# Optimization experiments

Measured on AMD Instinct MI355X. Metric: run time of the kernel, lower is better.

Reference implementation:

```python
import jax, jax.numpy as jnp
import numpy as np

B, F, D, V = 8192, 26, 32, 100000
H1, H2 = 128, 128  # cin_size
U1, U2 = 400, 400  # dnn hidden units


def setup_inputs() -> dict:
    key = jax.random.key(0)
    ks = jax.random.split(key, 12)
    s = 0.05  # keep activations/sigmoid in a sane range
    return {
        "dense_inputs": jax.random.normal(ks[0], (B, 13), jnp.float32),
        "sparse_inputs": jax.random.randint(ks[1], (B, F), 0, V, jnp.int32),
        "E": jax.random.normal(ks[2], (F, V, D), jnp.float32) * s,
        "W_cin0": jax.random.normal(ks[3], (F, F, H1), jnp.float32) * s,
        "W_cin1": jax.random.normal(ks[4], (F, H1, H2), jnp.float32) * s,
        "W1": jax.random.normal(ks[5], (F * D, U1), jnp.float32) * s,
        "b1": jnp.zeros((U1,), jnp.float32),
        "W2": jax.random.normal(ks[6], (U1, U2), jnp.float32) * s,
        "b2": jnp.zeros((U2,), jnp.float32),
        "w_lin": jax.random.normal(ks[7], (F, 1), jnp.float32) * s,
        "b_lin": jnp.zeros((1,), jnp.float32),
        "w_out": jax.random.normal(ks[8], (1 + H1 + H2 + U2 + 13, 1), jnp.float32) * s,
        "b_out": jnp.zeros((1,), jnp.float32),
    }


def reference(dense_inputs, sparse_inputs, E, W_cin0, W_cin1, W1, b1, W2, b2,
              w_lin, b_lin, w_out, b_out):
    # Linear part: Dense(1) applied to raw (cast) sparse ids, as in the TF code.
    linear_out = sparse_inputs.astype(jnp.float32) @ w_lin + b_lin  # [B,1]

    # Embedding lookup: per-field tables. embed[b,f,:] = E[f, sparse[b,f], :]
    embed = E[jnp.arange(F)[None, :], sparse_inputs]  # [B,F,D]

    # CIN. The split->matmul->reshape->conv1d chain is exactly:
    #   x_{k+1}[b,h,d] = sum_{i,j} W_k[i,j,h] * X0[b,i,d] * x_k[b,j,d]
    X0 = embed
    x1 = jnp.einsum('bid,bjd,ijh->bhd', X0, X0, W_cin0)   # [B,H1,D]
    x2 = jnp.einsum('bid,bjd,ijh->bhd', X0, x1, W_cin1)   # [B,H2,D]
    cin_out = jnp.concatenate([x1, x2], axis=1).sum(axis=-1)  # [B,H1+H2]

    # DNN on flattened embeddings (dropout rate 0 -> identity at inference).
    v = embed.reshape(B, F * D)
    h = jax.nn.relu(v @ W1 + b1)
    h = jax.nn.relu(h @ W2 + b2)  # [B,U2]

    total = jnp.concatenate([linear_out, cin_out, h, dense_inputs], axis=-1)
    return jax.nn.sigmoid(total @ w_out + b_out)  # [B,1]
```

## Files before the change

kernel.cpp:

```cpp
#include <hip/hip_runtime.h>
#include <hip/hip_bf16.h>
#include <math.h>

typedef __attribute__((ext_vector_type(8))) short bf16x8;
typedef __attribute__((ext_vector_type(4))) float f32x4;

#define B_ 8192
#define F_ 26
#define D_ 32
#define V_ 100000

static const size_t OFF_VB   = 0;
static const size_t OFF_FD0  = 13631488;
static const size_t OFF_PDH2 = 13664256;
static const size_t OFF_H1B  = 13795328;
static const size_t OFF_W1T  = 20348928;
static const size_t OFF_W2T  = 21014528;
static const size_t OFF_MTF  = 21334528;
static const size_t OFF_K2T  = 21350912;

static __device__ __forceinline__ unsigned short f2b(float f) {
    unsigned int u = __float_as_uint(f);
    return (unsigned short)((u + 0x7FFF + ((u >> 16) & 1)) >> 16);
}
static __device__ __forceinline__ unsigned short f2bt(float f) {
    return (unsigned short)(__float_as_uint(f) >> 16);
}
static __device__ __forceinline__ unsigned int pk2t(float a, float b) {
    return __builtin_amdgcn_perm(__float_as_uint(b), __float_as_uint(a), 0x07060302u);
}
static __device__ __forceinline__ float bf2f(unsigned short u) {
    return __uint_as_float(((unsigned int)u) << 16);
}

static __device__ __forceinline__ void transpose_body(
    const float* __restrict__ src, unsigned short* __restrict__ dst,
    int K, int N, int bx, int by)
{
    __shared__ float tl[32][33];
    const int lx = threadIdx.x & 31, ly = threadIdx.x >> 5;
    const int n0 = bx * 32, k0 = by * 32;
#pragma unroll
    for (int i = 0; i < 4; ++i) {
        int k = k0 + ly + i * 8, n = n0 + lx;
        if (k < K && n < N) tl[ly + i * 8][lx] = src[(size_t)k * N + n];
    }
    __syncthreads();
#pragma unroll
    for (int i = 0; i < 4; ++i) {
        int n = n0 + ly + i * 8, k = k0 + lx;
        if (k < K && n < N) dst[(size_t)n * K + k] = f2b(tl[lx][ly + i * 8]);
    }
}

__global__ __launch_bounds__(256) void k0a(
    const float* __restrict__ W1, const float* __restrict__ W2,
    const float* __restrict__ Wc1, const float* __restrict__ wout,
    unsigned short* __restrict__ W1t, unsigned short* __restrict__ W2t,
    float* __restrict__ MtF)
{
    __shared__ float w2s[128];
    int bid = blockIdx.x;
    if (bid < 338) { transpose_body(W1, W1t, 832, 400, bid % 13, bid / 13); return; }
    bid -= 338;
    if (bid < 169) { transpose_body(W2, W2t, 400, 400, bid % 13, bid / 13); return; }
    bid -= 169;
    if (threadIdx.x < 128) w2s[threadIdx.x] = wout[129 + threadIdx.x];
    __syncthreads();
    int g = bid * 256 + threadIdx.x;
    int i = g >> 7, j = g & 127;
    float s = 0.f;
    if (i < F_) {
        const float* row = Wc1 + ((size_t)i * 128 + j) * 128;
        for (int h = 0; h < 128; h += 4) {
            float4 a = *(const float4*)(row + h);
            s = fmaf(a.x, w2s[h], s);
            s = fmaf(a.y, w2s[h + 1], s);
            s = fmaf(a.z, w2s[h + 2], s);
            s = fmaf(a.w, w2s[h + 3], s);
        }
    } else if (i == F_) {
        s = wout[1 + j];
    }
    MtF[g] = s;
}

__global__ __launch_bounds__(256) void k0b(
    const float* __restrict__ W0, const float* __restrict__ MtF,
    unsigned short* __restrict__ K2T)
{
    int g = blockIdx.x * 256 + threadIdx.x;
    int q = g >> 5, i = g & 31;
    float s = 0.f;
    if (q < 351) {
        int a = 0, base = 0;
        while (base + (F_ - a) <= q) { base += F_ - a; ++a; }
        int b = a + (q - base);
        const float* r0 = W0 + ((size_t)a * F_ + b) * 128;
        const float* r1 = W0 + ((size_t)b * F_ + a) * 128;
        const float* m  = MtF + (size_t)i * 128;
        if (a == b) {
            for (int j = 0; j < 128; j += 4) {
                float4 w = *(const float4*)(r0 + j);
                float4 mm = *(const float4*)(m + j);
                s += w.x * mm.x + w.y * mm.y + w.z * mm.z + w.w * mm.w;
            }
        } else {
            for (int j = 0; j < 128; j += 4) {
                float4 w = *(const float4*)(r0 + j);
                float4 w1 = *(const float4*)(r1 + j);
                float4 mm = *(const float4*)(m + j);
                s += (w.x + w1.x) * mm.x + (w.y + w1.y) * mm.y
                   + (w.z + w1.z) * mm.z + (w.w + w1.w) * mm.w;
            }
        }
    }
    unsigned short hi = f2b(s);
    float lo = s - bf2f(hi);
    K2T[g] = hi;
    K2T[11264 + g] = f2b(lo);
}

__global__ __launch_bounds__(256) void k1_embed_cin(
    const int*   __restrict__ sparse,
    const float* __restrict__ E,
    const unsigned short* __restrict__ K2T,
    const float* __restrict__ wlin,
    const float* __restrict__ blin,
    const float* __restrict__ wout,
    unsigned short* __restrict__ vb,
    float* __restrict__ fdot0)
{
    __shared__ __align__(16) unsigned short embT[32][40];
    __shared__ unsigned int PQ[352];
    __shared__ int idxs[F_];
    __shared__ float red[4];

    const int b = blockIdx.x, t = threadIdx.x;
    float cind = 0.f;

    if (t < F_) {
        int id = sparse[b * F_ + t];
        idxs[t] = id;
        cind = (float)id * wlin[t] * wout[0];
        int base = F_ * t - (t * (t - 1)) / 2;
        for (int j = t; j < F_; ++j)
            PQ[base + j - t] = (unsigned)t | ((unsigned)j << 16);
    }
    if (t == F_) PQ[351] = 0u;
    if (t >= 32 && t < 64) {
        int d = t - 32;
        embT[d][26] = 0x3F80;
        embT[d][27] = 0; embT[d][28] = 0; embT[d][29] = 0;
        embT[d][30] = 0; embT[d][31] = 0;
    }
    __syncthreads();

    if (t < 208) {
        int f = t >> 3, q = t & 7;
        float4 v4 = *(const float4*)(E + ((size_t)f * V_ + idxs[f]) * D_ + q * 4);
        uint2 uu; uu.x = pk2t(v4.x, v4.y); uu.y = pk2t(v4.z, v4.w);
        *(uint2*)(vb + (size_t)b * 832 + f * 32 + q * 4) = uu;
        embT[q * 4 + 0][f] = f2bt(v4.x);
        embT[q * 4 + 1][f] = f2bt(v4.y);
        embT[q * 4 + 2][f] = f2bt(v4.z);
        embT[q * 4 + 3][f] = f2bt(v4.w);
    }
    __syncthreads();

    const int wave = t >> 6, lane = t & 63;
    const int lr = lane & 15, lg = lane >> 4;
    const int mt = wave & 1;
    const int nb = wave >> 1;
    bf16x8 af = *(const bf16x8*)&embT[mt * 16 + lr][lg * 8];
    const unsigned short* ebase = &embT[mt * 16 + lg * 4][0];
    const unsigned short* Kb = K2T + (size_t)lr * 32 + lg * 8;

#pragma unroll
    for (int s = 0; s < 11; ++s) {
        const int nt = 2 * s + nb;
        bf16x8 bh = *(const bf16x8*)(Kb + (size_t)nt * 512);
        bf16x8 bl = *(const bf16x8*)(Kb + 11264 + (size_t)nt * 512);
        f32x4 h = {};
        h = __builtin_amdgcn_mfma_f32_16x16x32_bf16(af, bl, h, 0, 0, 0);
        h = __builtin_amdgcn_mfma_f32_16x16x32_bf16(af, bh, h, 0, 0, 0);
        unsigned pq = PQ[nt * 16 + lr];
        int oi = (int)(pq & 0xFFFFu), oj = (int)(pq >> 16);
#pragma unroll
        for (int r = 0; r < 4; ++r) {
            float ei = bf2f(ebase[r * 40 + oi]);
            float ej = bf2f(ebase[r * 40 + oj]);
            cind = fmaf(ei * ej, h[r], cind);
        }
    }

#pragma unroll
    for (int off = 1; off <= 32; off <<= 1) cind += __shfl_xor(cind, off, 64);
    if (lane == 0) red[wave] = cind;
    __syncthreads();
    if (t == 0) fdot0[b] = red[0] + red[1] + red[2] + red[3] + blin[0] * wout[0];
}

static __device__ __forceinline__ void gemm_core(
    const unsigned short* __restrict__ A, int lda,
    const unsigned short* __restrict__ Bt, int ldb, int N,
    int m0, int n0, int kbase, int kend,
    unsigned short (*As)[40], unsigned short (*Bs)[40],
    f32x4 (*acc)[2])
{
    const int t = threadIdx.x;
    const int wave = t >> 6, lane = t & 63;
    const int lr = lane & 15, lg = lane >> 4;
    const int wn = wave * 32;
    const int ar = t >> 2, kg = (t & 3) * 8;

    const unsigned short* aptr = A  + (size_t)(m0 + ar) * lda + kbase + kg;
    const unsigned short* bp0  = Bt + (size_t)(n0 + ar) * ldb + kbase + kg;
    const unsigned short* bp1  = Bt + (size_t)(n0 + 64 + ar) * ldb + kbase + kg;
    const bool bn0 = (n0 + ar) < N, bn1 = (n0 + 64 + ar) < N;
    const uint4 z4 = make_uint4(0u, 0u, 0u, 0u);
    const int nkt = (kend - kbase + 31) >> 5;
    uint4 av, bv0, bv1;
    {
        int k = kbase + kg;
        av  = (k < kend)        ? *(const uint4*)aptr : z4;
        bv0 = (bn0 && k < kend) ? *(const uint4*)bp0  : z4;
        bv1 = (bn1 && k < kend) ? *(const uint4*)bp1  : z4;
    }
    for (int kt = 0; kt < nkt; ++kt) {
        *(uint4*)&As[ar][kg]      = av;
        *(uint4*)&Bs[ar][kg]      = bv0;
        *(uint4*)&Bs[64 + ar][kg] = bv1;
        __syncthreads();
        if (kt + 1 < nkt) {
            int kn = kbase + (kt + 1) * 32 + kg;
            av  = (kn < kend)        ? *(const uint4*)(aptr + (kt + 1) * 32) : z4;
            bv0 = (bn0 && kn < kend) ? *(const uint4*)(bp0  + (kt + 1) * 32) : z4;
            bv1 = (bn1 && kn < kend) ? *(const uint4*)(bp1  + (kt + 1) * 32) : z4;
        }
        bf16x8 af[4], bfr[2];
#pragma unroll
        for (int i = 0; i < 4; ++i) af[i]  = *(const bf16x8*)&As[i * 16 + lr][lg * 8];
#pragma unroll
        for (int j = 0; j < 2; ++j) bfr[j] = *(const bf16x8*)&Bs[wn + j * 16 + lr][lg * 8];
#pragma unroll
        for (int i = 0; i < 4; ++i)
#pragma unroll
            for (int j = 0; j < 2; ++j)
                acc[i][j] = __builtin_amdgcn_mfma_f32_16x16x32_bf16(af[i], bfr[j], acc[i][j], 0, 0, 0);
        __syncthreads();
    }
}

__global__ __launch_bounds__(256) void k2_h1(
    const unsigned short* __restrict__ vb, const unsigned short* __restrict__ W1t,
    const float* __restrict__ b1, unsigned short* __restrict__ h1b)
{
    __shared__ __align__(16) unsigned short As[64][40];
    __shared__ __align__(16) unsigned short Bs[128][40];
    const int t = threadIdx.x;
    const int wave = t >> 6, lane = t & 63;
    const int lr = lane & 15, lg = lane >> 4;
    const int m0 = blockIdx.y * 64, n0 = blockIdx.x * 128;
    f32x4 acc[4][2] = {};
    gemm_core(vb, 832, W1t, 832, 400, m0, n0, 0, 832, As, Bs, acc);
#pragma unroll
    for (int i = 0; i < 4; ++i) {
        int mrow = m0 + i * 16 + lg * 4;
#pragma unroll
        for (int j = 0; j < 2; ++j) {
            int col = n0 + wave * 32 + j * 16 + lr;
            if (col >= 400) continue;
            float bb = b1[col];
#pragma unroll
            for (int r = 0; r < 4; ++r)
                h1b[(size_t)(mrow + r) * 400 + col] = f2bt(fmaxf(acc[i][j][r] + bb, 0.f));
        }
    }
}

__global__ __launch_bounds__(256) void k2_h2(
    const unsigned short* __restrict__ h1b, const unsigned short* __restrict__ W2t,
    const float* __restrict__ b2, const float* __restrict__ wout,
    float* __restrict__ pdh2)
{
    __shared__ __align__(16) unsigned short As[64][40];
    __shared__ __align__(16) unsigned short Bs[128][40];
    __shared__ float red[4][64];
    const int t = threadIdx.x;
    const int wave = t >> 6, lane = t & 63;
    const int lr = lane & 15, lg = lane >> 4;
    const int m0 = blockIdx.y * 64, n0 = blockIdx.x * 128;
    f32x4 acc[4][2] = {};
    gemm_core(h1b, 400, W2t, 400, 400, m0, n0, 0, 400, As, Bs, acc);
    float v[4][4];
#pragma unroll
    for (int i = 0; i < 4; ++i)
#pragma unroll
        for (int r = 0; r < 4; ++r) {
            float s = 0.f;
#pragma unroll
            for (int j = 0; j < 2; ++j) {
                int col = n0 + wave * 32 + j * 16 + lr;
                if (col < 400)
                    s = fmaf(fmaxf(acc[i][j][r] + b2[col], 0.f), wout[257 + col], s);
            }
#pragma unroll
            for (int off = 1; off <= 8; off <<= 1) s += __shfl_xor(s, off, 64);
            v[i][r] = s;
        }
    if (lr == 0) {
#pragma unroll
        for (int i = 0; i < 4; ++i)
#pragma unroll
            for (int r = 0; r < 4; ++r) red[wave][i * 16 + lg * 4 + r] = v[i][r];
    }
    __syncthreads();
    if (t < 64) pdh2[(size_t)blockIdx.x * B_ + m0 + t] = red[0][t] + red[1][t] + red[2][t] + red[3][t];
}

__global__ __launch_bounds__(256) void k3_final(
    const float* __restrict__ fdot0,
    const float* __restrict__ pdh2,
    const float* __restrict__ dense,
    const float* __restrict__ wout,
    const float* __restrict__ bout,
    float* __restrict__ out)
{
    const int b = blockIdx.x * 256 + threadIdx.x;
    float s = fdot0[b];
#pragma unroll
    for (int z = 0; z < 4; ++z) s += pdh2[(size_t)z * B_ + b];
#pragma unroll
    for (int q = 0; q < 13; ++q) s = fmaf(dense[(size_t)b * 13 + q], wout[657 + q], s);
    out[b] = 1.f / (1.f + expf(-(s + bout[0])));
}

extern "C" void kernel_launch(void* const* d_in, const int* in_sizes, int n_in,
                              void* d_out, int out_size, void* d_ws, size_t ws_size,
                              hipStream_t stream) {
    const float* dense  = (const float*)d_in[0];
    const int*   sparse = (const int*)  d_in[1];
    const float* E      = (const float*)d_in[2];
    const float* W0     = (const float*)d_in[3];
    const float* Wc1    = (const float*)d_in[4];
    const float* W1     = (const float*)d_in[5];
    const float* b1     = (const float*)d_in[6];
    const float* W2     = (const float*)d_in[7];
    const float* b2     = (const float*)d_in[8];
    const float* wlin   = (const float*)d_in[9];
    const float* blin   = (const float*)d_in[10];
    const float* wout   = (const float*)d_in[11];
    const float* bout   = (const float*)d_in[12];
    float* out = (float*)d_out;

    char* ws = (char*)d_ws;
    unsigned short* vb    = (unsigned short*)(ws + OFF_VB);
    float*          fdot0 = (float*)(ws + OFF_FD0);
    float*          pdh2  = (float*)(ws + OFF_PDH2);
    unsigned short* h1b   = (unsigned short*)(ws + OFF_H1B);
    unsigned short* W1t   = (unsigned short*)(ws + OFF_W1T);
    unsigned short* W2t   = (unsigned short*)(ws + OFF_W2T);
    float*          MtF   = (float*)(ws + OFF_MTF);
    unsigned short* K2T   = (unsigned short*)(ws + OFF_K2T);

    k0a<<<338 + 169 + 16, 256, 0, stream>>>(W1, W2, Wc1, wout, W1t, W2t, MtF);
    k0b<<<44, 256, 0, stream>>>(W0, MtF, K2T);
    k1_embed_cin<<<B_, 256, 0, stream>>>(sparse, E, K2T, wlin, blin, wout, vb, fdot0);
    k2_h1<<<dim3(4, 128), 256, 0, stream>>>(vb, W1t, b1, h1b);
    k2_h2<<<dim3(4, 128), 256, 0, stream>>>(h1b, W2t, b2, wout, pdh2);
    k3_final<<<B_ / 256, 256, 0, stream>>>(fdot0, pdh2, dense, wout, bout, out);
}
```

Before: 491.3 us.

## Merge weight-prep kernels and fuse second DNN layer with final sigmoid

Two changes. The two preprocessing kernels are folded into one: each block now computes one row of the CIN Wc1·w_out product into shared memory and then produces its column of K2T, so the MtF intermediate buffer and one launch go away. The second DNN GEMM, previously tiled 64x128 with partial dot products written to a pdh2 buffer and reduced by a separate final kernel, becomes a 32-row-per-block kernel. It keeps the whole h1 row slice in LDS, streams W2t directly from global memory into MFMA, and finishes with the dot product, dense term and sigmoid in place. This removes two launches and the pdh2 round trip, but the layer-2 grid shrinks to 256 blocks and W2t is re-read from global/L2 by every block without LDS staging.

```diff
diff --git a/kernel.cpp b/kernel.cpp
--- a/kernel.cpp
+++ b/kernel.cpp
@@ -12,12 +12,10 @@
 
 static const size_t OFF_VB   = 0;
 static const size_t OFF_FD0  = 13631488;
-static const size_t OFF_PDH2 = 13664256;
-static const size_t OFF_H1B  = 13795328;
-static const size_t OFF_W1T  = 20348928;
-static const size_t OFF_W2T  = 21014528;
-static const size_t OFF_MTF  = 21334528;
-static const size_t OFF_K2T  = 21350912;
+static const size_t OFF_H1B  = 13664256;
+static const size_t OFF_W1T  = 20217856;
+static const size_t OFF_W2T  = 20883456;
+static const size_t OFF_K2T  = 21203456;
 
 static __device__ __forceinline__ unsigned short f2b(float f) {
     unsigned int u = __float_as_uint(f);
@@ -53,72 +51,65 @@
     }
 }
 
-__global__ __launch_bounds__(256) void k0a(
+__global__ __launch_bounds__(256) void k0_all(
     const float* __restrict__ W1, const float* __restrict__ W2,
-    const float* __restrict__ Wc1, const float* __restrict__ wout,
+    const float* __restrict__ W0, const float* __restrict__ Wc1,
+    const float* __restrict__ wout,
     unsigned short* __restrict__ W1t, unsigned short* __restrict__ W2t,
-    float* __restrict__ MtF)
-{
-    __shared__ float w2s[128];
+    unsigned short* __restrict__ K2T)
+{
+    __shared__ float Mi[128];
     int bid = blockIdx.x;
+    const int t = threadIdx.x;
     if (bid < 338) { transpose_body(W1, W1t, 832, 400, bid % 13, bid / 13); return; }
     bid -= 338;
     if (bid < 169) { transpose_body(W2, W2t, 400, 400, bid % 13, bid / 13); return; }
     bid -= 169;
-    if (threadIdx.x < 128) w2s[threadIdx.x] = wout[129 + threadIdx.x];
-    __syncthreads();
-    int g = bid * 256 + threadIdx.x;
-    int i = g >> 7, j = g & 127;
-    float s = 0.f;
-    if (i < F_) {
-        const float* row = Wc1 + ((size_t)i * 128 + j) * 128;
-        for (int h = 0; h < 128; h += 4) {
-            float4 a = *(const float4*)(row + h);
-            s = fmaf(a.x, w2s[h], s);
-            s = fmaf(a.y, w2s[h + 1], s);
-            s = fmaf(a.z, w2s[h + 2], s);
-            s = fmaf(a.w, w2s[h + 3], s);
-        }
-    } else if (i == F_) {
-        s = wout[1 + j];
-    }
-    MtF[g] = s;
-}
-
-__global__ __launch_bounds__(256) void k0b(
-    const float* __restrict__ W0, const float* __restrict__ MtF,
-    unsigned short* __restrict__ K2T)
-{
-    int g = blockIdx.x * 256 + threadIdx.x;
-    int q = g >> 5, i = g & 31;
-    float s = 0.f;
-    if (q < 351) {
-        int a = 0, base = 0;
-        while (base + (F_ - a) <= q) { base += F_ - a; ++a; }
-        int b = a + (q - base);
-        const float* r0 = W0 + ((size_t)a * F_ + b) * 128;
-        const float* r1 = W0 + ((size_t)b * F_ + a) * 128;
-        const float* m  = MtF + (size_t)i * 128;
-        if (a == b) {
-            for (int j = 0; j < 128; j += 4) {
-                float4 w = *(const float4*)(r0 + j);
-                float4 mm = *(const float4*)(m + j);
-                s += w.x * mm.x + w.y * mm.y + w.z * mm.z + w.w * mm.w;
+    const int i = bid;
+    if (t < 128) {
+        float m = 0.f;
+        if (i < F_) {
+            const float* row = Wc1 + ((size_t)i * 128 + t) * 128;
+            for (int h = 0; h < 128; h += 4) {
+                float4 a = *(const float4*)(row + h);
+                m = fmaf(a.x, wout[129 + h],     m);
+                m = fmaf(a.y, wout[129 + h + 1], m);
+                m = fmaf(a.z, wout[129 + h + 2], m);
+                m = fmaf(a.w, wout[129 + h + 3], m);
             }
-        } else {
-            for (int j = 0; j < 128; j += 4) {
-                float4 w = *(const float4*)(r0 + j);
-                float4 w1 = *(const float4*)(r1 + j);
-                float4 mm = *(const float4*)(m + j);
-                s += (w.x + w1.x) * mm.x + (w.y + w1.y) * mm.y
-                   + (w.z + w1.z) * mm.z + (w.w + w1.w) * mm.w;
+        } else if (i == F_) {
+            m = wout[1 + t];
+        }
+        Mi[t] = m;
+    }
+    __syncthreads();
+    for (int q = t; q < 352; q += 256) {
+        float s = 0.f;
+        if (q < 351 && i <= F_) {
+            int a = 0, base = 0;
+            while (base + (F_ - a) <= q) { base += F_ - a; ++a; }
+            int b = a + (q - base);
+            const float* r0 = W0 + ((size_t)a * F_ + b) * 128;
+            const float* r1 = W0 + ((size_t)b * F_ + a) * 128;
+            if (a == b) {
+                for (int j = 0; j < 128; j += 4) {
+                    float4 w = *(const float4*)(r0 + j);
+                    s += w.x * Mi[j] + w.y * Mi[j + 1] + w.z * Mi[j + 2] + w.w * Mi[j + 3];
+                }
+            } else {
+                for (int j = 0; j < 128; j += 4) {
+                    float4 w  = *(const float4*)(r0 + j);
+                    float4 w1 = *(const float4*)(r1 + j);
+                    s += (w.x + w1.x) * Mi[j]     + (w.y + w1.y) * Mi[j + 1]
+                       + (w.z + w1.z) * Mi[j + 2] + (w.w + w1.w) * Mi[j + 3];
+                }
             }
         }
-    }
-    unsigned short hi = f2b(s);
-    float lo = s - bf2f(hi);
-    K2T[g] = hi;
-    K2T[11264 + g] = f2b(lo);
+        unsigned short hi = f2b(s);
+        float lo = s - bf2f(hi);
+        K2T[q * 32 + i] = hi;
+        K2T[11264 + q * 32 + i] = f2b(lo);
+    }
 }
 
 __global__ __launch_bounds__(256) void k1_embed_cin(
@@ -279,61 +270,74 @@
     }
 }
 
-__global__ __launch_bounds__(256) void k2_h2(
+__global__ __launch_bounds__(256) void k2_h2f(
     const unsigned short* __restrict__ h1b, const unsigned short* __restrict__ W2t,
     const float* __restrict__ b2, const float* __restrict__ wout,
-    float* __restrict__ pdh2)
-{
-    __shared__ __align__(16) unsigned short As[64][40];
-    __shared__ __align__(16) unsigned short Bs[128][40];
-    __shared__ float red[4][64];
+    const float* __restrict__ fdot0, const float* __restrict__ dense,
+    const float* __restrict__ bout, float* __restrict__ out)
+{
+    __shared__ __align__(16) unsigned short As[32][424];
+    __shared__ float red[4][32];
     const int t = threadIdx.x;
+    const int m0 = blockIdx.x * 32;
+
+    for (int idx = t; idx < 1600; idx += 256) {
+        int row = idx / 50, c = idx - row * 50;
+        *(uint4*)&As[row][c * 8] = *(const uint4*)(h1b + (size_t)(m0 + row) * 400 + c * 8);
+    }
+    if (t < 96) {
+        int row = t / 3, c = t - row * 3;
+        uint4 z = make_uint4(0u, 0u, 0u, 0u);
+        *(uint4*)&As[row][400 + c * 8] = z;
+    }
+    __syncthreads();
+
     const int wave = t >> 6, lane = t & 63;
     const int lr = lane & 15, lg = lane >> 4;
-    const int m0 = blockIdx.y * 64, n0 = blockIdx.x * 128;
-    f32x4 acc[4][2] = {};
-    gemm_core(h1b, 400, W2t, 400, 400, m0, n0, 0, 400, As, Bs, acc);
-    float v[4][4];
-#pragma unroll
-    for (int i = 0; i < 4; ++i)
+    float s[2][4] = {};
+
+    for (int nt = wave; nt < 25; nt += 4) {
+        f32x4 acc0 = {}, acc1 = {};
+        const unsigned short* bp = W2t + (size_t)(nt * 16 + lr) * 400 + lg * 8;
+#pragma unroll
+        for (int kt = 0; kt < 13; ++kt) {
+            const int kk = kt * 32 + lg * 8;
+            bf16x8 bw = {};
+            if (kk < 400) bw = *(const bf16x8*)(bp + kt * 32);
+            bf16x8 a0 = *(const bf16x8*)&As[lr][kk];
+            bf16x8 a1 = *(const bf16x8*)&As[16 + lr][kk];
+            acc0 = __builtin_amdgcn_mfma_f32_16x16x32_bf16(a0, bw, acc0, 0, 0, 0);
+            acc1 = __builtin_amdgcn_mfma_f32_16x16x32_bf16(a1, bw, acc1, 0, 0, 0);
+        }
+        const int col = nt * 16 + lr;
+        const float bb = b2[col], wo = wout[257 + col];
 #pragma unroll
         for (int r = 0; r < 4; ++r) {
-            float s = 0.f;
-#pragma unroll
-            for (int j = 0; j < 2; ++j) {
-                int col = n0 + wave * 32 + j * 16 + lr;
-                if (col < 400)
-                    s = fmaf(fmaxf(acc[i][j][r] + b2[col], 0.f), wout[257 + col], s);
-            }
-#pragma unroll
-            for (int off = 1; off <= 8; off <<= 1) s += __shfl_xor(s, off, 64);
-            v[i][r] = s;
-        }
-    if (lr == 0) {
-#pragma unroll
-        for (int i = 0; i < 4; ++i)
-#pragma unroll
-            for (int r = 0; r < 4; ++r) red[wave][i * 16 + lg * 4 + r] = v[i][r];
-    }
-    __syncthreads();
-    if (t < 64) pdh2[(size_t)blockIdx.x * B_ + m0 + t] = red[0][t] + red[1][t] + red[2][t] + red[3][t];
-}
-
-__global__ __launch_bounds__(256) void k3_final(
-    const float* __restrict__ fdot0,
-    const float* __restrict__ pdh2,
-    const float* __restrict__ dense,
-    const float* __restrict__ wout,
-    const float* __restrict__ bout,
-    float* __restrict__ out)
-{
-    const int b = blockIdx.x * 256 + threadIdx.x;
-    float s = fdot0[b];
-#pragma unroll
-    for (int z = 0; z < 4; ++z) s += pdh2[(size_t)z * B_ + b];
-#pragma unroll
-    for (int q = 0; q < 13; ++q) s = fmaf(dense[(size_t)b * 13 + q], wout[657 + q], s);
-    out[b] = 1.f / (1.f + expf(-(s + bout[0])));
+            s[0][r] = fmaf(fmaxf(acc0[r] + bb, 0.f), wo, s[0][r]);
+            s[1][r] = fmaf(fmaxf(acc1[r] + bb, 0.f), wo, s[1][r]);
+        }
+    }
+#pragma unroll
+    for (int mt = 0; mt < 2; ++mt)
+#pragma unroll
+        for (int r = 0; r < 4; ++r) {
+            float v = s[mt][r];
+            v += __shfl_xor(v, 1, 64);
+            v += __shfl_xor(v, 2, 64);
+            v += __shfl_xor(v, 4, 64);
+            v += __shfl_xor(v, 8, 64);
+            if (lr == 0) red[wave][mt * 16 + lg * 4 + r] = v;
+        }
+    __syncthreads();
+    if (t < 32) {
+        const int b = m0 + t;
+        float tot = red[0][t] + red[1][t] + red[2][t] + red[3][t]
+                  + fdot0[b] + bout[0];
+#pragma unroll
+        for (int q = 0; q < 13; ++q)
+            tot = fmaf(dense[(size_t)b * 13 + q], wout[657 + q], tot);
+        out[b] = 1.f / (1.f + expf(-tot));
+    }
 }
 
 extern "C" void kernel_launch(void* const* d_in, const int* in_sizes, int n_in,
@@ -357,17 +361,13 @@
     char* ws = (char*)d_ws;
     unsigned short* vb    = (unsigned short*)(ws + OFF_VB);
     float*          fdot0 = (float*)(ws + OFF_FD0);
-    float*          pdh2  = (float*)(ws + OFF_PDH2);
     unsigned short* h1b   = (unsigned short*)(ws + OFF_H1B);
     unsigned short* W1t   = (unsigned short*)(ws + OFF_W1T);
     unsigned short* W2t   = (unsigned short*)(ws + OFF_W2T);
-    float*          MtF   = (float*)(ws + OFF_MTF);
     unsigned short* K2T   = (unsigned short*)(ws + OFF_K2T);
 
-    k0a<<<338 + 169 + 16, 256, 0, stream>>>(W1, W2, Wc1, wout, W1t, W2t, MtF);
-    k0b<<<44, 256, 0, stream>>>(W0, MtF, K2T);
+    k0_all<<<338 + 169 + 32, 256, 0, stream>>>(W1, W2, W0, Wc1, wout, W1t, W2t, K2T);
     k1_embed_cin<<<B_, 256, 0, stream>>>(sparse, E, K2T, wlin, blin, wout, vb, fdot0);
     k2_h1<<<dim3(4, 128), 256, 0, stream>>>(vb, W1t, b1, h1b);
-    k2_h2<<<dim3(4, 128), 256, 0, stream>>>(h1b, W2t, b2, wout, pdh2);
-    k3_final<<<B_ / 256, 256, 0, stream>>>(fdot0, pdh2, dense, wout, bout, out);
-}
+    k2_h2f<<<256, 256, 0, stream>>>(h1b, W2t, b2, wout, fdot0, dense, bout, out);
+}
```

New measurement: 510.9 us. 4.0% more time.
